# Performance work log

Hardware: AMD Instinct MI355X
Metric: run time of the kernel (lower is better)

Reference implementation:

```python
import jax, jax.numpy as jnp
import numpy as np

N_USERS = 100_000
N_ITEMS = 50_000
N = N_USERS + N_ITEMS
N_LAYERS = 3
ALPHA = 0.8
D = 64
IMG_D = 4096
TXT_D = 384
N_INTER = 2_000_000  # user-item interactions; symmetric nnz = 2*N_INTER


def setup_inputs() -> dict:
    # --- build symmetric-normalized bipartite adjacency (D^-1/2 A D^-1/2) in numpy ---
    rng = np.random.default_rng(0)
    u = rng.integers(0, N_USERS, N_INTER).astype(np.int32)
    i = (rng.integers(0, N_ITEMS, N_INTER) + N_USERS).astype(np.int32)
    rows = np.concatenate([u, i])
    cols = np.concatenate([i, u])
    deg = np.bincount(rows, minlength=N).astype(np.float32)
    d_inv = np.where(deg > 0, deg ** -0.5, 0.0).astype(np.float32)
    vals = d_inv[rows] * d_inv[cols]

    key = jax.random.key(0)
    ks = jax.random.split(key, 8)
    xav_img = float(np.sqrt(6.0 / (IMG_D + D)))
    xav_txt = float(np.sqrt(6.0 / (TXT_D + D)))
    return {
        "image_feats": jax.random.normal(ks[0], (N_ITEMS, IMG_D), jnp.float32),
        "text_feats": jax.random.normal(ks[1], (N_ITEMS, TXT_D), jnp.float32),
        "image_pref": jax.random.normal(ks[2], (N_USERS, D), jnp.float32),
        "text_pref": jax.random.normal(ks[3], (N_USERS, D), jnp.float32),
        "W_img": jax.random.uniform(ks[4], (IMG_D, D), jnp.float32, -xav_img, xav_img),
        "b_img": jnp.zeros((D,), jnp.float32),
        "W_txt": jax.random.uniform(ks[5], (TXT_D, D), jnp.float32, -xav_txt, xav_txt),
        "b_txt": jnp.zeros((D,), jnp.float32),
        "adj_vals": jnp.asarray(vals),
        "adj_rows": jnp.asarray(rows),
        "adj_cols": jnp.asarray(cols),
    }


def _spmm(rows, cols, vals, x):
    # sparse COO @ dense: out[r] += vals[e] * x[cols[e]]
    return jax.ops.segment_sum(vals[:, None] * x[cols], rows, num_segments=N)


def _l2norm(x):
    # F.normalize(x, dim=1): row-wise L2 with eps clamp
    return x / jnp.clip(jnp.linalg.norm(x, axis=1, keepdims=True), 1e-12)


def reference(image_feats, text_feats, image_pref, text_pref,
              W_img, b_img, W_txt, b_txt, adj_vals, adj_rows, adj_cols):
    img = _l2norm(image_feats @ W_img + b_img)   # [n_items, D]
    txt = _l2norm(text_feats @ W_txt + b_txt)    # [n_items, D]
    ego_i = jnp.concatenate([image_pref, img], axis=0)  # [N, D]
    ego_t = jnp.concatenate([text_pref, txt], axis=0)   # [N, D]
    for _ in range(N_LAYERS):
        ego_i = _spmm(adj_rows, adj_cols, adj_vals, ego_i) + ALPHA * ego_i
        ego_t = _spmm(adj_rows, adj_cols, adj_vals, ego_t) + ALPHA * ego_t
    user_preference = jnp.concatenate([ego_i[:N_USERS], ego_t[:N_USERS]], axis=1)  # [n_users, 2D]
    items = jnp.concatenate([ego_i[N_USERS:], ego_t[N_USERS:]], axis=1)            # [n_items, 2D]
    return user_preference, items
```

## Files before the change

### kernel.cpp

```cpp
#include <hip/hip_runtime.h>
#include <hip/hip_bf16.h>

#define N_USERS 100000
#define N_ITEMS 50000
#define N_TOTAL 150000
#define NNZ     4000000
#define ALPHA_F 0.8f
#define ELL_CAP 128

#define G_GEMM 782
#define G_COPY 256
#define G_SCAT 1024
#define NC_IMG 64
#define NC_ALL 70

typedef __attribute__((ext_vector_type(8))) short bf16x8;
typedef __attribute__((ext_vector_type(4))) float f32x4;

static __device__ __forceinline__ short f2bf(float f) {
    unsigned u = __builtin_bit_cast(unsigned, f);
    unsigned r = (u + 0x7fff + ((u >> 16) & 1)) >> 16;
    return (short)r;
}
static __device__ __forceinline__ unsigned pack_bf2(float a, float b) {
    return (unsigned)(unsigned short)f2bf(a) | ((unsigned)(unsigned short)f2bf(b) << 16);
}
static __device__ __forceinline__ float bf_lo(unsigned u) { return __uint_as_float(u << 16); }
static __device__ __forceinline__ float bf_hi(unsigned u) { return __uint_as_float(u & 0xFFFF0000u); }

static __device__ __forceinline__ void gload_lds16(const void* src, void* dst) {
    __builtin_amdgcn_global_load_lds(
        (const __attribute__((address_space(1))) unsigned*)src,
        (__attribute__((address_space(3))) unsigned*)dst, 16, 0, 0);
}


__global__ __launch_bounds__(256) void prep_kernel(const float* __restrict__ Wimg,
                                                   const float* __restrict__ Wtxt,
                                                   int* __restrict__ cnt,
                                                   short* __restrict__ Wti,
                                                   short* __restrict__ Wtt) {
    const int T0 = N_TOTAL;
    const int T1 = T0 + 4096 * 64;
    const int T2 = T1 + 384 * 64;
    int i = blockIdx.x * 256 + threadIdx.x;
    int stride = gridDim.x * 256;
    for (; i < T2; i += stride) {
        if (i < T0) {
            cnt[i] = 0;
        } else if (i < T1) {
            int idx = i - T0; int k = idx >> 6, n = idx & 63;
            Wti[(size_t)n * 4096 + k] = f2bf(Wimg[(size_t)k * 64 + n]);
        } else {
            int idx = i - T1; int k = idx >> 6, n = idx & 63;
            Wtt[(size_t)n * 384 + k] = f2bf(Wtxt[(size_t)k * 64 + n]);
        }
    }
}


static __device__ __forceinline__ void compute_chunk(
        const float* at, const short* bt, int wave, int lane,
        f32x4& c0, f32x4& c1, f32x4& c2, f32x4& c3) {
    const int col = lane & 15, kb = lane >> 4;
    const int arow = 16 * wave + col;
    const char* abase = (const char*)at + arow * 256;
    const int aswz = (arow & 7) << 4;
    const int bswz = (col & 7) << 4;
    const char* bb = (const char*)bt;
    #pragma unroll
    for (int ks = 0; ks < 2; ++ks) {
        int Xa = ks * 128 + kb * 32;
        float4 a0v = *(const float4*)(abase + ((Xa)      ^ aswz));
        float4 a1v = *(const float4*)(abase + ((Xa + 16) ^ aswz));
        bf16x8 af;
        af[0]=f2bf(a0v.x); af[1]=f2bf(a0v.y); af[2]=f2bf(a0v.z); af[3]=f2bf(a0v.w);
        af[4]=f2bf(a1v.x); af[5]=f2bf(a1v.y); af[6]=f2bf(a1v.z); af[7]=f2bf(a1v.w);
        int xb = (ks * 64 + kb * 16) ^ bswz;
        bf16x8 b0 = *(const bf16x8*)(bb + (col +  0) * 128 + xb);
        bf16x8 b1 = *(const bf16x8*)(bb + (col + 16) * 128 + xb);
        bf16x8 b2 = *(const bf16x8*)(bb + (col + 32) * 128 + xb);
        bf16x8 b3 = *(const bf16x8*)(bb + (col + 48) * 128 + xb);
        c0 = __builtin_amdgcn_mfma_f32_16x16x32_bf16(af, b0, c0, 0, 0, 0);
        c1 = __builtin_amdgcn_mfma_f32_16x16x32_bf16(af, b1, c1, 0, 0, 0);
        c2 = __builtin_amdgcn_mfma_f32_16x16x32_bf16(af, b2, c2, 0, 0, 0);
        c3 = __builtin_amdgcn_mfma_f32_16x16x32_bf16(af, b3, c3, 0, 0, 0);
    }
}


__global__ __launch_bounds__(256) void mega_kernel(
        const float* __restrict__ Aimg, const float* __restrict__ Atxt,
        const short* __restrict__ Wti, const short* __restrict__ Wtt,
        const float* __restrict__ bimg, const float* __restrict__ btxt,
        unsigned* __restrict__ egob,
        const int* __restrict__ rows, const int* __restrict__ cols,
        const float* __restrict__ vals, int* __restrict__ cnt, int2* __restrict__ ell,
        const float* __restrict__ img_pref, const float* __restrict__ txt_pref) {
    __shared__ __align__(16) float atile[2][64 * 64];
    __shared__ __align__(16) short btile[2][64 * 64];
    int b = blockIdx.x;
    int t = threadIdx.x;
    int wave = t >> 6, lane = t & 63;
    if (b < G_GEMM) {
        const int row0 = b * 64;
        const int gmax = N_ITEMS - 1;
        const int col = lane & 15, kb = lane >> 4;

        auto stageA = [&](const float* A, int K, int k0, int bi) {
            #pragma unroll
            for (int c = 0; c < 4; ++c) {
                int g = c * 4 + wave;
                int r = g * 4 + (lane >> 4);
                int gr = row0 + r; gr = gr > gmax ? gmax : gr;
                int boff = ((lane & 15) * 16) ^ ((r & 7) << 4);
                const char* src = (const char*)A + ((size_t)gr * K + k0) * 4 + boff;
                char* dst = (char*)&atile[bi][0] + g * 1024 + lane * 16;
                gload_lds16(src, dst);
            }
        };
        auto stageB = [&](const short* W, int K, int k0, int bi) {
            #pragma unroll
            for (int c = 0; c < 2; ++c) {
                int g = c * 4 + wave;
                int bc = g * 8 + (lane >> 3);
                int boff = ((lane & 7) * 16) ^ ((bc & 7) << 4);
                const char* src = (const char*)W + ((size_t)bc * K + k0) * 2 + boff;
                char* dst = (char*)&btile[bi][0] + g * 1024 + lane * 16;
                gload_lds16(src, dst);
            }
        };
        auto stage = [&](int ci, int bi) {
            if (ci < NC_IMG) { stageA(Aimg, 4096, ci * 64, bi); stageB(Wti, 4096, ci * 64, bi); }
            else { stageA(Atxt, 384, (ci - NC_IMG) * 64, bi); stageB(Wtt, 384, (ci - NC_IMG) * 64, bi); }
        };

        f32x4 z = {0.f,0.f,0.f,0.f};
        f32x4 ai0 = z, ai1 = z, ai2 = z, ai3 = z;
        f32x4 at0 = z, at1 = z, at2 = z, at3 = z;

        stage(0, 0);
        for (int ci = 0; ci < NC_ALL; ++ci) {
            int bi = ci & 1;
            if (ci + 1 < NC_ALL) {
                stage(ci + 1, bi ^ 1);
                asm volatile("s_waitcnt vmcnt(6)" ::: "memory");
            } else {
                asm volatile("s_waitcnt vmcnt(0)" ::: "memory");
            }
            __builtin_amdgcn_s_barrier();
            __builtin_amdgcn_sched_barrier(0);
            if (ci < NC_IMG) compute_chunk(&atile[bi][0], &btile[bi][0], wave, lane, ai0, ai1, ai2, ai3);
            else             compute_chunk(&atile[bi][0], &btile[bi][0], wave, lane, at0, at1, at2, at3);
            asm volatile("" ::: "memory");
            __builtin_amdgcn_s_barrier();
            __builtin_amdgcn_sched_barrier(0);
        }

        float bi0 = bimg[ 0 + col], bi1 = bimg[16 + col], bi2 = bimg[32 + col], bi3 = bimg[48 + col];
        float bt0 = btxt[ 0 + col], bt1 = btxt[16 + col], bt2 = btxt[32 + col], bt3 = btxt[48 + col];
        #pragma unroll
        for (int i = 0; i < 4; ++i) {
            ai0[i] += bi0; ai1[i] += bi1; ai2[i] += bi2; ai3[i] += bi3;
            at0[i] += bt0; at1[i] += bt1; at2[i] += bt2; at3[i] += bt3;
        }
        unsigned* egob_items = egob + (size_t)N_USERS * 64;
        #pragma unroll
        for (int i = 0; i < 4; ++i) {
            float ssi = ai0[i]*ai0[i] + ai1[i]*ai1[i] + ai2[i]*ai2[i] + ai3[i]*ai3[i];
            float sst = at0[i]*at0[i] + at1[i]*at1[i] + at2[i]*at2[i] + at3[i]*at3[i];
            #pragma unroll
            for (int off = 1; off < 16; off <<= 1) {
                ssi += __shfl_xor(ssi, off, 64);
                sst += __shfl_xor(sst, off, 64);
            }
            float rni = 1.0f / fmaxf(sqrtf(ssi), 1e-12f);
            float rnt = 1.0f / fmaxf(sqrtf(sst), 1e-12f);
            int r = row0 + 16 * wave + kb * 4 + i;
            if (r < N_ITEMS) {
                unsigned* ob = egob_items + (size_t)r * 64 + col;
                ob[ 0] = pack_bf2(ai0[i]*rni, at0[i]*rnt);
                ob[16] = pack_bf2(ai1[i]*rni, at1[i]*rnt);
                ob[32] = pack_bf2(ai2[i]*rni, at2[i]*rnt);
                ob[48] = pack_bf2(ai3[i]*rni, at3[i]*rnt);
            }
        }
    } else if (b < G_GEMM + G_COPY) {
        int idx = (b - G_GEMM) * 256 + t;
        int stride = G_COPY * 256;
        for (; idx < N_USERS * 16; idx += stride) {
            int row = idx >> 4, w4 = (idx & 15) << 2;
            float4 iv = *reinterpret_cast<const float4*>(&img_pref[(size_t)row * 64 + w4]);
            float4 tv = *reinterpret_cast<const float4*>(&txt_pref[(size_t)row * 64 + w4]);
            uint4 m;
            m.x = pack_bf2(iv.x, tv.x); m.y = pack_bf2(iv.y, tv.y);
            m.z = pack_bf2(iv.z, tv.z); m.w = pack_bf2(iv.w, tv.w);
            *reinterpret_cast<uint4*>(&egob[(size_t)row * 64 + w4]) = m;
        }
    } else {
        int i = (b - G_GEMM - G_COPY) * 256 + t;
        int stride = G_SCAT * 256;
        for (; i < NNZ; i += stride) {
            int r = rows[i];
            int p = atomicAdd(&cnt[r], 1);
            if (p < ELL_CAP)
                ell[(size_t)r * ELL_CAP + p] = make_int2(cols[i], __float_as_int(vals[i]));
        }
    }
}


__global__ __launch_bounds__(256) void spmm_sort_kernel(
        const int* __restrict__ cnt, int2* __restrict__ ell,
        const unsigned* __restrict__ xb, unsigned* __restrict__ outb) {
    __shared__ __align__(16) int2 srt[4][ELL_CAP];
    int wid = threadIdx.x >> 6, lane = threadIdx.x & 63;
    int row = blockIdx.x * 4 + wid;
    bool valid = row < N_TOTAL;
    int deg = 0;
    int2* base = nullptr;
    int2 e0 = make_int2(0x7FFFFFFF, 0), e1 = e0;
    if (valid) {
        deg = min(cnt[row], ELL_CAP);
        base = ell + (size_t)row * ELL_CAP;
        if (lane < deg)      e0 = base[lane];
        if (lane + 64 < deg) e1 = base[lane + 64];
    }
    #pragma unroll
    for (int k = 2; k <= 128; k <<= 1) {
        #pragma unroll
        for (int j = 64; j >= 1; j >>= 1) {
            if (j >= k) continue;
            if (j == 64) {
                if (e0.x > e1.x) { int2 tmp = e0; e0 = e1; e1 = tmp; }
            } else {
                int2 p0, p1;
                p0.x = __shfl_xor(e0.x, j, 64); p0.y = __shfl_xor(e0.y, j, 64);
                p1.x = __shfl_xor(e1.x, j, 64); p1.y = __shfl_xor(e1.y, j, 64);
                bool up0 = ((lane & k) == 0);
                bool up1 = (((lane + 64) & k) == 0);
                bool lo0 = ((lane & j) == 0);
                bool keepmin0 = (up0 == lo0);
                bool keepmin1 = (up1 == lo0);
                if (keepmin0 ? (e0.x > p0.x) : (e0.x < p0.x)) e0 = p0;
                if (keepmin1 ? (e1.x > p1.x) : (e1.x < p1.x)) e1 = p1;
            }
        }
    }
    if (valid) {
        if (lane < deg)      base[lane]      = e0;
        if (lane + 64 < deg) base[lane + 64] = e1;
    }
    srt[wid][lane] = e0;
    srt[wid][lane + 64] = e1;
    __syncthreads();
    if (!valid) return;
    unsigned sw = xb[(size_t)row * 64 + lane];
    float2 acc;
    acc.x = ALPHA_F * bf_lo(sw);
    acc.y = ALPHA_F * bf_hi(sw);
    const int2* s = srt[wid];
    int i = 0;
    for (; i + 8 <= deg; i += 8) {
        int4 p0 = *reinterpret_cast<const int4*>(s + i);
        int4 p1 = *reinterpret_cast<const int4*>(s + i + 2);
        int4 p2 = *reinterpret_cast<const int4*>(s + i + 4);
        int4 p3 = *reinterpret_cast<const int4*>(s + i + 6);
        unsigned g0 = xb[(size_t)p0.x * 64 + lane];
        unsigned g1 = xb[(size_t)p0.z * 64 + lane];
        unsigned g2 = xb[(size_t)p1.x * 64 + lane];
        unsigned g3 = xb[(size_t)p1.z * 64 + lane];
        unsigned g4 = xb[(size_t)p2.x * 64 + lane];
        unsigned g5 = xb[(size_t)p2.z * 64 + lane];
        unsigned g6 = xb[(size_t)p3.x * 64 + lane];
        unsigned g7 = xb[(size_t)p3.z * 64 + lane];
        float v0 = __int_as_float(p0.y), v1 = __int_as_float(p0.w);
        float v2 = __int_as_float(p1.y), v3 = __int_as_float(p1.w);
        float v4 = __int_as_float(p2.y), v5 = __int_as_float(p2.w);
        float v6 = __int_as_float(p3.y), v7 = __int_as_float(p3.w);
        acc.x = fmaf(v0, bf_lo(g0), acc.x); acc.y = fmaf(v0, bf_hi(g0), acc.y);
        acc.x = fmaf(v1, bf_lo(g1), acc.x); acc.y = fmaf(v1, bf_hi(g1), acc.y);
        acc.x = fmaf(v2, bf_lo(g2), acc.x); acc.y = fmaf(v2, bf_hi(g2), acc.y);
        acc.x = fmaf(v3, bf_lo(g3), acc.x); acc.y = fmaf(v3, bf_hi(g3), acc.y);
        acc.x = fmaf(v4, bf_lo(g4), acc.x); acc.y = fmaf(v4, bf_hi(g4), acc.y);
        acc.x = fmaf(v5, bf_lo(g5), acc.x); acc.y = fmaf(v5, bf_hi(g5), acc.y);
        acc.x = fmaf(v6, bf_lo(g6), acc.x); acc.y = fmaf(v6, bf_hi(g6), acc.y);
        acc.x = fmaf(v7, bf_lo(g7), acc.x); acc.y = fmaf(v7, bf_hi(g7), acc.y);
    }
    for (; i < deg; ++i) {
        int2 c = s[i];
        float v = __int_as_float(c.y);
        unsigned g = xb[(size_t)c.x * 64 + lane];
        acc.x = fmaf(v, bf_lo(g), acc.x);
        acc.y = fmaf(v, bf_hi(g), acc.y);
    }
    outb[(size_t)row * 64 + lane] = pack_bf2(acc.x, acc.y);
}


__global__ __launch_bounds__(256) void spmm_kernel(
        const int* __restrict__ cnt, const int2* __restrict__ ell,
        const unsigned* __restrict__ xb,
        float* __restrict__ out32, unsigned* __restrict__ outb) {
    int row = blockIdx.x * 4 + (threadIdx.x >> 6);
    if (row >= N_TOTAL) return;
    int lane = threadIdx.x & 63;
    unsigned sw = xb[(size_t)row * 64 + lane];
    float2 acc;
    acc.x = ALPHA_F * bf_lo(sw);
    acc.y = ALPHA_F * bf_hi(sw);
    int deg = min(cnt[row], ELL_CAP);
    const int2* base = ell + (size_t)row * ELL_CAP;
    int i = 0;
    for (; i + 8 <= deg; i += 8) {
        int4 p0 = *reinterpret_cast<const int4*>(base + i);
        int4 p1 = *reinterpret_cast<const int4*>(base + i + 2);
        int4 p2 = *reinterpret_cast<const int4*>(base + i + 4);
        int4 p3 = *reinterpret_cast<const int4*>(base + i + 6);
        unsigned g0 = xb[(size_t)p0.x * 64 + lane];
        unsigned g1 = xb[(size_t)p0.z * 64 + lane];
        unsigned g2 = xb[(size_t)p1.x * 64 + lane];
        unsigned g3 = xb[(size_t)p1.z * 64 + lane];
        unsigned g4 = xb[(size_t)p2.x * 64 + lane];
        unsigned g5 = xb[(size_t)p2.z * 64 + lane];
        unsigned g6 = xb[(size_t)p3.x * 64 + lane];
        unsigned g7 = xb[(size_t)p3.z * 64 + lane];
        float v0 = __int_as_float(p0.y), v1 = __int_as_float(p0.w);
        float v2 = __int_as_float(p1.y), v3 = __int_as_float(p1.w);
        float v4 = __int_as_float(p2.y), v5 = __int_as_float(p2.w);
        float v6 = __int_as_float(p3.y), v7 = __int_as_float(p3.w);
        acc.x = fmaf(v0, bf_lo(g0), acc.x); acc.y = fmaf(v0, bf_hi(g0), acc.y);
        acc.x = fmaf(v1, bf_lo(g1), acc.x); acc.y = fmaf(v1, bf_hi(g1), acc.y);
        acc.x = fmaf(v2, bf_lo(g2), acc.x); acc.y = fmaf(v2, bf_hi(g2), acc.y);
        acc.x = fmaf(v3, bf_lo(g3), acc.x); acc.y = fmaf(v3, bf_hi(g3), acc.y);
        acc.x = fmaf(v4, bf_lo(g4), acc.x); acc.y = fmaf(v4, bf_hi(g4), acc.y);
        acc.x = fmaf(v5, bf_lo(g5), acc.x); acc.y = fmaf(v5, bf_hi(g5), acc.y);
        acc.x = fmaf(v6, bf_lo(g6), acc.x); acc.y = fmaf(v6, bf_hi(g6), acc.y);
        acc.x = fmaf(v7, bf_lo(g7), acc.x); acc.y = fmaf(v7, bf_hi(g7), acc.y);
    }
    for (; i < deg; ++i) {
        int2 c = base[i];
        float v = __int_as_float(c.y);
        unsigned g = xb[(size_t)c.x * 64 + lane];
        acc.x = fmaf(v, bf_lo(g), acc.x);
        acc.y = fmaf(v, bf_hi(g), acc.y);
    }
    if (out32) {
        out32[(size_t)row * 128 + lane] = acc.x;
        out32[(size_t)row * 128 + 64 + lane] = acc.y;
    }
    if (outb)
        outb[(size_t)row * 64 + lane] = pack_bf2(acc.x, acc.y);
}


extern "C" void kernel_launch(void* const* d_in, const int* in_sizes, int n_in,
                              void* d_out, int out_size, void* d_ws, size_t ws_size,
                              hipStream_t stream) {
    const float* image_feats = (const float*)d_in[0];
    const float* text_feats  = (const float*)d_in[1];
    const float* image_pref  = (const float*)d_in[2];
    const float* text_pref   = (const float*)d_in[3];
    const float* W_img       = (const float*)d_in[4];
    const float* b_img       = (const float*)d_in[5];
    const float* W_txt       = (const float*)d_in[6];
    const float* b_txt       = (const float*)d_in[7];
    const float* adj_vals    = (const float*)d_in[8];
    const int*   adj_rows    = (const int*)d_in[9];
    const int*   adj_cols    = (const int*)d_in[10];

    float* out = (float*)d_out;

    char* ws = (char*)d_ws;
    size_t off = 0;
    auto alloc = [&](size_t bytes) { char* p = ws + off; off += (bytes + 255) & ~size_t(255); return p; };
    int*      cnt    = (int*)     alloc(N_TOTAL * sizeof(int));
    int2*     ell    = (int2*)    alloc((size_t)N_TOTAL * ELL_CAP * sizeof(int2));
    unsigned* m0     = (unsigned*)alloc((size_t)N_TOTAL * 64 * sizeof(unsigned));
    unsigned* m1     = (unsigned*)alloc((size_t)N_TOTAL * 64 * sizeof(unsigned));
    short*    Wt_img = (short*)   alloc((size_t)64 * 4096 * sizeof(short));
    short*    Wt_txt = (short*)   alloc((size_t)64 * 384 * sizeof(short));
    (void)ws_size; (void)out_size; (void)n_in; (void)in_sizes;

    prep_kernel<<<512, 256, 0, stream>>>(W_img, W_txt, cnt, Wt_img, Wt_txt);

    mega_kernel<<<G_GEMM + G_COPY + G_SCAT, 256, 0, stream>>>(
        image_feats, text_feats, Wt_img, Wt_txt, b_img, b_txt, m0,
        adj_rows, adj_cols, adj_vals, cnt, ell, image_pref, text_pref);

    const int ROW_GRID = (N_TOTAL + 3) / 4;
    spmm_sort_kernel<<<ROW_GRID, 256, 0, stream>>>(cnt, ell, m0, m1);
    spmm_kernel<<<ROW_GRID, 256, 0, stream>>>(cnt, ell, m1, nullptr, m0);
    spmm_kernel<<<ROW_GRID, 256, 0, stream>>>(cnt, ell, m0, out, nullptr);
}
```

Baseline: 995.7 us.

## Retile projection GEMM to 16-row blocks with weights read from global

```diff
diff --git a/kernel.cpp b/kernel.cpp
--- a/kernel.cpp
+++ b/kernel.cpp
@@ -8,11 +8,10 @@
 #define ALPHA_F 0.8f
 #define ELL_CAP 128
 
-#define G_GEMM 782
-#define G_COPY 256
-#define G_SCAT 1024
-#define NC_IMG 64
-#define NC_ALL 70
+#define G_SCAT 256
+#define G_COPY 128
+#define G_PRE  (G_SCAT + G_COPY)
+#define G_GEMM 3125
 
 typedef __attribute__((ext_vector_type(8))) short bf16x8;
 typedef __attribute__((ext_vector_type(4))) float f32x4;
@@ -59,37 +58,7 @@
 }
 
 
-static __device__ __forceinline__ void compute_chunk(
-        const float* at, const short* bt, int wave, int lane,
-        f32x4& c0, f32x4& c1, f32x4& c2, f32x4& c3) {
-    const int col = lane & 15, kb = lane >> 4;
-    const int arow = 16 * wave + col;
-    const char* abase = (const char*)at + arow * 256;
-    const int aswz = (arow & 7) << 4;
-    const int bswz = (col & 7) << 4;
-    const char* bb = (const char*)bt;
-    #pragma unroll
-    for (int ks = 0; ks < 2; ++ks) {
-        int Xa = ks * 128 + kb * 32;
-        float4 a0v = *(const float4*)(abase + ((Xa)      ^ aswz));
-        float4 a1v = *(const float4*)(abase + ((Xa + 16) ^ aswz));
-        bf16x8 af;
-        af[0]=f2bf(a0v.x); af[1]=f2bf(a0v.y); af[2]=f2bf(a0v.z); af[3]=f2bf(a0v.w);
-        af[4]=f2bf(a1v.x); af[5]=f2bf(a1v.y); af[6]=f2bf(a1v.z); af[7]=f2bf(a1v.w);
-        int xb = (ks * 64 + kb * 16) ^ bswz;
-        bf16x8 b0 = *(const bf16x8*)(bb + (col +  0) * 128 + xb);
-        bf16x8 b1 = *(const bf16x8*)(bb + (col + 16) * 128 + xb);
-        bf16x8 b2 = *(const bf16x8*)(bb + (col + 32) * 128 + xb);
-        bf16x8 b3 = *(const bf16x8*)(bb + (col + 48) * 128 + xb);
-        c0 = __builtin_amdgcn_mfma_f32_16x16x32_bf16(af, b0, c0, 0, 0, 0);
-        c1 = __builtin_amdgcn_mfma_f32_16x16x32_bf16(af, b1, c1, 0, 0, 0);
-        c2 = __builtin_amdgcn_mfma_f32_16x16x32_bf16(af, b2, c2, 0, 0, 0);
-        c3 = __builtin_amdgcn_mfma_f32_16x16x32_bf16(af, b3, c3, 0, 0, 0);
-    }
-}
-
-
-__global__ __launch_bounds__(256) void mega_kernel(
+__global__ __launch_bounds__(256, 4) void mega_kernel(
         const float* __restrict__ Aimg, const float* __restrict__ Atxt,
         const short* __restrict__ Wti, const short* __restrict__ Wtt,
         const float* __restrict__ bimg, const float* __restrict__ btxt,
@@ -97,96 +66,24 @@
         const int* __restrict__ rows, const int* __restrict__ cols,
         const float* __restrict__ vals, int* __restrict__ cnt, int2* __restrict__ ell,
         const float* __restrict__ img_pref, const float* __restrict__ txt_pref) {
-    __shared__ __align__(16) float atile[2][64 * 64];
-    __shared__ __align__(16) short btile[2][64 * 64];
+    __shared__ __align__(16) char atile[32768];
     int b = blockIdx.x;
     int t = threadIdx.x;
     int wave = t >> 6, lane = t & 63;
-    if (b < G_GEMM) {
-        const int row0 = b * 64;
-        const int gmax = N_ITEMS - 1;
-        const int col = lane & 15, kb = lane >> 4;
-
-        auto stageA = [&](const float* A, int K, int k0, int bi) {
-            #pragma unroll
-            for (int c = 0; c < 4; ++c) {
-                int g = c * 4 + wave;
-                int r = g * 4 + (lane >> 4);
-                int gr = row0 + r; gr = gr > gmax ? gmax : gr;
-                int boff = ((lane & 15) * 16) ^ ((r & 7) << 4);
-                const char* src = (const char*)A + ((size_t)gr * K + k0) * 4 + boff;
-                char* dst = (char*)&atile[bi][0] + g * 1024 + lane * 16;
-                gload_lds16(src, dst);
-            }
-        };
-        auto stageB = [&](const short* W, int K, int k0, int bi) {
-            #pragma unroll
-            for (int c = 0; c < 2; ++c) {
-                int g = c * 4 + wave;
-                int bc = g * 8 + (lane >> 3);
-                int boff = ((lane & 7) * 16) ^ ((bc & 7) << 4);
-                const char* src = (const char*)W + ((size_t)bc * K + k0) * 2 + boff;
-                char* dst = (char*)&btile[bi][0] + g * 1024 + lane * 16;
-                gload_lds16(src, dst);
-            }
-        };
-        auto stage = [&](int ci, int bi) {
-            if (ci < NC_IMG) { stageA(Aimg, 4096, ci * 64, bi); stageB(Wti, 4096, ci * 64, bi); }
-            else { stageA(Atxt, 384, (ci - NC_IMG) * 64, bi); stageB(Wtt, 384, (ci - NC_IMG) * 64, bi); }
-        };
-
-        f32x4 z = {0.f,0.f,0.f,0.f};
-        f32x4 ai0 = z, ai1 = z, ai2 = z, ai3 = z;
-        f32x4 at0 = z, at1 = z, at2 = z, at3 = z;
-
-        stage(0, 0);
-        for (int ci = 0; ci < NC_ALL; ++ci) {
-            int bi = ci & 1;
-            if (ci + 1 < NC_ALL) {
-                stage(ci + 1, bi ^ 1);
-                asm volatile("s_waitcnt vmcnt(6)" ::: "memory");
-            } else {
-                asm volatile("s_waitcnt vmcnt(0)" ::: "memory");
-            }
-            __builtin_amdgcn_s_barrier();
-            __builtin_amdgcn_sched_barrier(0);
-            if (ci < NC_IMG) compute_chunk(&atile[bi][0], &btile[bi][0], wave, lane, ai0, ai1, ai2, ai3);
-            else             compute_chunk(&atile[bi][0], &btile[bi][0], wave, lane, at0, at1, at2, at3);
-            asm volatile("" ::: "memory");
-            __builtin_amdgcn_s_barrier();
-            __builtin_amdgcn_sched_barrier(0);
-        }
-
-        float bi0 = bimg[ 0 + col], bi1 = bimg[16 + col], bi2 = bimg[32 + col], bi3 = bimg[48 + col];
-        float bt0 = btxt[ 0 + col], bt1 = btxt[16 + col], bt2 = btxt[32 + col], bt3 = btxt[48 + col];
-        #pragma unroll
-        for (int i = 0; i < 4; ++i) {
-            ai0[i] += bi0; ai1[i] += bi1; ai2[i] += bi2; ai3[i] += bi3;
-            at0[i] += bt0; at1[i] += bt1; at2[i] += bt2; at3[i] += bt3;
-        }
-        unsigned* egob_items = egob + (size_t)N_USERS * 64;
-        #pragma unroll
-        for (int i = 0; i < 4; ++i) {
-            float ssi = ai0[i]*ai0[i] + ai1[i]*ai1[i] + ai2[i]*ai2[i] + ai3[i]*ai3[i];
-            float sst = at0[i]*at0[i] + at1[i]*at1[i] + at2[i]*at2[i] + at3[i]*at3[i];
-            #pragma unroll
-            for (int off = 1; off < 16; off <<= 1) {
-                ssi += __shfl_xor(ssi, off, 64);
-                sst += __shfl_xor(sst, off, 64);
-            }
-            float rni = 1.0f / fmaxf(sqrtf(ssi), 1e-12f);
-            float rnt = 1.0f / fmaxf(sqrtf(sst), 1e-12f);
-            int r = row0 + 16 * wave + kb * 4 + i;
-            if (r < N_ITEMS) {
-                unsigned* ob = egob_items + (size_t)r * 64 + col;
-                ob[ 0] = pack_bf2(ai0[i]*rni, at0[i]*rnt);
-                ob[16] = pack_bf2(ai1[i]*rni, at1[i]*rnt);
-                ob[32] = pack_bf2(ai2[i]*rni, at2[i]*rnt);
-                ob[48] = pack_bf2(ai3[i]*rni, at3[i]*rnt);
-            }
-        }
-    } else if (b < G_GEMM + G_COPY) {
-        int idx = (b - G_GEMM) * 256 + t;
+
+    if (b < G_SCAT) {
+        int i = b * 256 + t;
+        int stride = G_SCAT * 256;
+        for (; i < NNZ; i += stride) {
+            int r = rows[i];
+            int p = atomicAdd(&cnt[r], 1);
+            if (p < ELL_CAP)
+                ell[(size_t)r * ELL_CAP + p] = make_int2(cols[i], __float_as_int(vals[i]));
+        }
+        return;
+    }
+    if (b < G_PRE) {
+        int idx = (b - G_SCAT) * 256 + t;
         int stride = G_COPY * 256;
         for (; idx < N_USERS * 16; idx += stride) {
             int row = idx >> 4, w4 = (idx & 15) << 2;
@@ -197,15 +94,127 @@
             m.z = pack_bf2(iv.z, tv.z); m.w = pack_bf2(iv.w, tv.w);
             *reinterpret_cast<uint4*>(&egob[(size_t)row * 64 + w4]) = m;
         }
-    } else {
-        int i = (b - G_GEMM - G_COPY) * 256 + t;
-        int stride = G_SCAT * 256;
-        for (; i < NNZ; i += stride) {
-            int r = rows[i];
-            int p = atomicAdd(&cnt[r], 1);
-            if (p < ELL_CAP)
-                ell[(size_t)r * ELL_CAP + p] = make_int2(cols[i], __float_as_int(vals[i]));
-        }
+        return;
+    }
+
+    const int blk = b - G_PRE;
+    const int row0 = blk * 16;
+    const int col = lane & 15, kb = lane >> 4;
+
+    auto stage_img = [&](int ci, int bi) {
+        #pragma unroll
+        for (int j = 0; j < 4; ++j) {
+            int r = wave * 4 + j;
+            int swz = (r & 7) << 4;
+            const char* src = (const char*)Aimg + (size_t)(row0 + r) * 16384
+                              + ci * 1024 + ((lane * 16) ^ swz);
+            char* dst = (char*)atile + bi * 16384 + r * 1024;
+            gload_lds16(src, dst);
+        }
+    };
+    auto stage_txt1 = [&](int bi) {
+        #pragma unroll
+        for (int j = 0; j < 4; ++j) {
+            int r = wave * 4 + j;
+            int swz = (r & 7) << 4;
+            const char* src = (const char*)Atxt + (size_t)(row0 + r) * 1536
+                              + ((lane * 16) ^ swz);
+            char* dst = (char*)atile + bi * 16384 + r * 1024;
+            gload_lds16(src, dst);
+        }
+    };
+    auto stage_txt2 = [&](int bi) {
+        #pragma unroll
+        for (int j = 0; j < 2; ++j) {
+            int p = wave * 2 + j;
+            int r = p * 2 + (lane >> 5);
+            int swz = (r & 7) << 4;
+            const char* src = (const char*)Atxt + (size_t)(row0 + r) * 1536
+                              + 1024 + (((lane & 31) * 16) ^ swz);
+            char* dst = (char*)atile + bi * 16384 + p * 1024;
+            gload_lds16(src, dst);
+        }
+    };
+    auto comp = [&](const char* base, int rstride, const short* Wt, int K, int kabs,
+                    int nks, f32x4& acc) {
+        const int row = col;
+        const int swz = (row & 7) << 4;
+        const char* ab = base + row * rstride;
+        const short* wp = Wt + (size_t)(16 * wave + col) * K + kabs + kb * 8;
+        for (int ks = 0; ks < nks; ++ks) {
+            int lg = kb * 32 + ks * 128;
+            float4 a0 = *(const float4*)(ab + (lg ^ swz));
+            float4 a1 = *(const float4*)(ab + ((lg + 16) ^ swz));
+            bf16x8 af;
+            af[0]=f2bf(a0.x); af[1]=f2bf(a0.y); af[2]=f2bf(a0.z); af[3]=f2bf(a0.w);
+            af[4]=f2bf(a1.x); af[5]=f2bf(a1.y); af[6]=f2bf(a1.z); af[7]=f2bf(a1.w);
+            bf16x8 bf = *(const bf16x8*)(wp + ks * 32);
+            acc = __builtin_amdgcn_mfma_f32_16x16x32_bf16(af, bf, acc, 0, 0, 0);
+        }
+    };
+
+    f32x4 ai = {0.f,0.f,0.f,0.f}, at4 = {0.f,0.f,0.f,0.f};
+
+    stage_img(0, 0);
+    for (int ci = 0; ci < 16; ++ci) {
+        int bi = ci & 1;
+        if (ci < 15) stage_img(ci + 1, bi ^ 1);
+        else         stage_txt1(bi ^ 1);
+        asm volatile("s_waitcnt vmcnt(4)" ::: "memory");
+        __builtin_amdgcn_s_barrier();
+        __builtin_amdgcn_sched_barrier(0);
+        comp((const char*)atile + bi * 16384, 1024, Wti, 4096, ci * 256, 8, ai);
+        asm volatile("" ::: "memory");
+        __builtin_amdgcn_s_barrier();
+        __builtin_amdgcn_sched_barrier(0);
+    }
+    stage_txt2(1);
+    asm volatile("s_waitcnt vmcnt(2)" ::: "memory");
+    __builtin_amdgcn_s_barrier();
+    __builtin_amdgcn_sched_barrier(0);
+    comp((const char*)atile, 1024, Wtt, 384, 0, 8, at4);
+    asm volatile("s_waitcnt vmcnt(0)" ::: "memory");
+    __builtin_amdgcn_s_barrier();
+    __builtin_amdgcn_sched_barrier(0);
+    comp((const char*)atile + 16384, 512, Wtt, 384, 256, 4, at4);
+
+    float bv_i = bimg[16 * wave + col];
+    float bv_t = btxt[16 * wave + col];
+    float ssi[4], sst[4];
+    #pragma unroll
+    for (int i = 0; i < 4; ++i) {
+        ai[i] += bv_i; at4[i] += bv_t;
+        ssi[i] = ai[i] * ai[i];
+        sst[i] = at4[i] * at4[i];
+    }
+    #pragma unroll
+    for (int off = 1; off < 16; off <<= 1) {
+        #pragma unroll
+        for (int i = 0; i < 4; ++i) {
+            ssi[i] += __shfl_xor(ssi[i], off, 64);
+            sst[i] += __shfl_xor(sst[i], off, 64);
+        }
+    }
+    float* S = (float*)atile;
+    __syncthreads();
+    if (col == 0) {
+        #pragma unroll
+        for (int i = 0; i < 4; ++i) {
+            S[wave * 16 + kb * 4 + i]      = ssi[i];
+            S[64 + wave * 16 + kb * 4 + i] = sst[i];
+        }
+    }
+    __syncthreads();
+    unsigned* egob_items = egob + (size_t)N_USERS * 64;
+    #pragma unroll
+    for (int i = 0; i < 4; ++i) {
+        int r = kb * 4 + i;
+        float ti = S[r] + S[16 + r] + S[32 + r] + S[48 + r];
+        float tt = S[64 + r] + S[80 + r] + S[96 + r] + S[112 + r];
+        float rni = 1.0f / fmaxf(sqrtf(ti), 1e-12f);
+        float rnt = 1.0f / fmaxf(sqrtf(tt), 1e-12f);
+        egob_items[(size_t)(row0 + r) * 64 + 16 * wave + col] =
+            pack_bf2(ai[i] * rni, at4[i] * rnt);
     }
 }
 
@@ -384,7 +393,7 @@
 
     prep_kernel<<<512, 256, 0, stream>>>(W_img, W_txt, cnt, Wt_img, Wt_txt);
 
-    mega_kernel<<<G_GEMM + G_COPY + G_SCAT, 256, 0, stream>>>(
+    mega_kernel<<<G_PRE + G_GEMM, 256, 0, stream>>>(
         image_feats, text_feats, Wt_img, Wt_txt, b_img, b_txt, m0,
         adj_rows, adj_cols, adj_vals, cnt, ell, image_pref, text_pref);
 
```

Measured after the change: 976.3 us. No clear change (-1.9%).

## Reorder mega kernel blocks, pre-tile swizzled weights, add occupancy hint

Applied to the files above, without the earlier changes.

```diff
diff --git a/kernel.cpp b/kernel.cpp
--- a/kernel.cpp
+++ b/kernel.cpp
@@ -8,9 +8,10 @@
 #define ALPHA_F 0.8f
 #define ELL_CAP 128
 
+#define G_SCAT 1024
+#define G_COPY 128
+#define G_PRE  (G_SCAT + G_COPY)
 #define G_GEMM 782
-#define G_COPY 256
-#define G_SCAT 1024
 #define NC_IMG 64
 #define NC_ALL 70
 
@@ -38,8 +39,8 @@
 __global__ __launch_bounds__(256) void prep_kernel(const float* __restrict__ Wimg,
                                                    const float* __restrict__ Wtxt,
                                                    int* __restrict__ cnt,
-                                                   short* __restrict__ Wti,
-                                                   short* __restrict__ Wtt) {
+                                                   char* __restrict__ WtiT,
+                                                   char* __restrict__ WttT) {
     const int T0 = N_TOTAL;
     const int T1 = T0 + 4096 * 64;
     const int T2 = T1 + 384 * 64;
@@ -50,143 +51,46 @@
             cnt[i] = 0;
         } else if (i < T1) {
             int idx = i - T0; int k = idx >> 6, n = idx & 63;
-            Wti[(size_t)n * 4096 + k] = f2bf(Wimg[(size_t)k * 64 + n]);
+            int c = k >> 6, kk = k & 63;
+            *(short*)(WtiT + c * 8192 + n * 128 + ((kk * 2) ^ ((n & 7) << 4)))
+                = f2bf(Wimg[(size_t)k * 64 + n]);
         } else {
             int idx = i - T1; int k = idx >> 6, n = idx & 63;
-            Wtt[(size_t)n * 384 + k] = f2bf(Wtxt[(size_t)k * 64 + n]);
-        }
-    }
-}
-
-
-static __device__ __forceinline__ void compute_chunk(
-        const float* at, const short* bt, int wave, int lane,
-        f32x4& c0, f32x4& c1, f32x4& c2, f32x4& c3) {
-    const int col = lane & 15, kb = lane >> 4;
-    const int arow = 16 * wave + col;
-    const char* abase = (const char*)at + arow * 256;
-    const int aswz = (arow & 7) << 4;
-    const int bswz = (col & 7) << 4;
-    const char* bb = (const char*)bt;
-    #pragma unroll
-    for (int ks = 0; ks < 2; ++ks) {
-        int Xa = ks * 128 + kb * 32;
-        float4 a0v = *(const float4*)(abase + ((Xa)      ^ aswz));
-        float4 a1v = *(const float4*)(abase + ((Xa + 16) ^ aswz));
-        bf16x8 af;
-        af[0]=f2bf(a0v.x); af[1]=f2bf(a0v.y); af[2]=f2bf(a0v.z); af[3]=f2bf(a0v.w);
-        af[4]=f2bf(a1v.x); af[5]=f2bf(a1v.y); af[6]=f2bf(a1v.z); af[7]=f2bf(a1v.w);
-        int xb = (ks * 64 + kb * 16) ^ bswz;
-        bf16x8 b0 = *(const bf16x8*)(bb + (col +  0) * 128 + xb);
-        bf16x8 b1 = *(const bf16x8*)(bb + (col + 16) * 128 + xb);
-        bf16x8 b2 = *(const bf16x8*)(bb + (col + 32) * 128 + xb);
-        bf16x8 b3 = *(const bf16x8*)(bb + (col + 48) * 128 + xb);
-        c0 = __builtin_amdgcn_mfma_f32_16x16x32_bf16(af, b0, c0, 0, 0, 0);
-        c1 = __builtin_amdgcn_mfma_f32_16x16x32_bf16(af, b1, c1, 0, 0, 0);
-        c2 = __builtin_amdgcn_mfma_f32_16x16x32_bf16(af, b2, c2, 0, 0, 0);
-        c3 = __builtin_amdgcn_mfma_f32_16x16x32_bf16(af, b3, c3, 0, 0, 0);
-    }
-}
-
-
-__global__ __launch_bounds__(256) void mega_kernel(
+            int c = k >> 6, kk = k & 63;
+            *(short*)(WttT + c * 8192 + n * 128 + ((kk * 2) ^ ((n & 7) << 4)))
+                = f2bf(Wtxt[(size_t)k * 64 + n]);
+        }
+    }
+}
+
+
+__global__ __launch_bounds__(256, 3) void mega_kernel(
         const float* __restrict__ Aimg, const float* __restrict__ Atxt,
-        const short* __restrict__ Wti, const short* __restrict__ Wtt,
+        const char* __restrict__ WtiT, const char* __restrict__ WttT,
         const float* __restrict__ bimg, const float* __restrict__ btxt,
         unsigned* __restrict__ egob,
         const int* __restrict__ rows, const int* __restrict__ cols,
         const float* __restrict__ vals, int* __restrict__ cnt, int2* __restrict__ ell,
         const float* __restrict__ img_pref, const float* __restrict__ txt_pref) {
-    __shared__ __align__(16) float atile[2][64 * 64];
-    __shared__ __align__(16) short btile[2][64 * 64];
+    __shared__ __align__(16) char abuf[2][16384];
+    __shared__ __align__(16) char bbuf[2][8192];
     int b = blockIdx.x;
     int t = threadIdx.x;
     int wave = t >> 6, lane = t & 63;
-    if (b < G_GEMM) {
-        const int row0 = b * 64;
-        const int gmax = N_ITEMS - 1;
-        const int col = lane & 15, kb = lane >> 4;
-
-        auto stageA = [&](const float* A, int K, int k0, int bi) {
-            #pragma unroll
-            for (int c = 0; c < 4; ++c) {
-                int g = c * 4 + wave;
-                int r = g * 4 + (lane >> 4);
-                int gr = row0 + r; gr = gr > gmax ? gmax : gr;
-                int boff = ((lane & 15) * 16) ^ ((r & 7) << 4);
-                const char* src = (const char*)A + ((size_t)gr * K + k0) * 4 + boff;
-                char* dst = (char*)&atile[bi][0] + g * 1024 + lane * 16;
-                gload_lds16(src, dst);
-            }
-        };
-        auto stageB = [&](const short* W, int K, int k0, int bi) {
-            #pragma unroll
-            for (int c = 0; c < 2; ++c) {
-                int g = c * 4 + wave;
-                int bc = g * 8 + (lane >> 3);
-                int boff = ((lane & 7) * 16) ^ ((bc & 7) << 4);
-                const char* src = (const char*)W + ((size_t)bc * K + k0) * 2 + boff;
-                char* dst = (char*)&btile[bi][0] + g * 1024 + lane * 16;
-                gload_lds16(src, dst);
-            }
-        };
-        auto stage = [&](int ci, int bi) {
-            if (ci < NC_IMG) { stageA(Aimg, 4096, ci * 64, bi); stageB(Wti, 4096, ci * 64, bi); }
-            else { stageA(Atxt, 384, (ci - NC_IMG) * 64, bi); stageB(Wtt, 384, (ci - NC_IMG) * 64, bi); }
-        };
-
-        f32x4 z = {0.f,0.f,0.f,0.f};
-        f32x4 ai0 = z, ai1 = z, ai2 = z, ai3 = z;
-        f32x4 at0 = z, at1 = z, at2 = z, at3 = z;
-
-        stage(0, 0);
-        for (int ci = 0; ci < NC_ALL; ++ci) {
-            int bi = ci & 1;
-            if (ci + 1 < NC_ALL) {
-                stage(ci + 1, bi ^ 1);
-                asm volatile("s_waitcnt vmcnt(6)" ::: "memory");
-            } else {
-                asm volatile("s_waitcnt vmcnt(0)" ::: "memory");
-            }
-            __builtin_amdgcn_s_barrier();
-            __builtin_amdgcn_sched_barrier(0);
-            if (ci < NC_IMG) compute_chunk(&atile[bi][0], &btile[bi][0], wave, lane, ai0, ai1, ai2, ai3);
-            else             compute_chunk(&atile[bi][0], &btile[bi][0], wave, lane, at0, at1, at2, at3);
-            asm volatile("" ::: "memory");
-            __builtin_amdgcn_s_barrier();
-            __builtin_amdgcn_sched_barrier(0);
-        }
-
-        float bi0 = bimg[ 0 + col], bi1 = bimg[16 + col], bi2 = bimg[32 + col], bi3 = bimg[48 + col];
-        float bt0 = btxt[ 0 + col], bt1 = btxt[16 + col], bt2 = btxt[32 + col], bt3 = btxt[48 + col];
-        #pragma unroll
-        for (int i = 0; i < 4; ++i) {
-            ai0[i] += bi0; ai1[i] += bi1; ai2[i] += bi2; ai3[i] += bi3;
-            at0[i] += bt0; at1[i] += bt1; at2[i] += bt2; at3[i] += bt3;
-        }
-        unsigned* egob_items = egob + (size_t)N_USERS * 64;
-        #pragma unroll
-        for (int i = 0; i < 4; ++i) {
-            float ssi = ai0[i]*ai0[i] + ai1[i]*ai1[i] + ai2[i]*ai2[i] + ai3[i]*ai3[i];
-            float sst = at0[i]*at0[i] + at1[i]*at1[i] + at2[i]*at2[i] + at3[i]*at3[i];
-            #pragma unroll
-            for (int off = 1; off < 16; off <<= 1) {
-                ssi += __shfl_xor(ssi, off, 64);
-                sst += __shfl_xor(sst, off, 64);
-            }
-            float rni = 1.0f / fmaxf(sqrtf(ssi), 1e-12f);
-            float rnt = 1.0f / fmaxf(sqrtf(sst), 1e-12f);
-            int r = row0 + 16 * wave + kb * 4 + i;
-            if (r < N_ITEMS) {
-                unsigned* ob = egob_items + (size_t)r * 64 + col;
-                ob[ 0] = pack_bf2(ai0[i]*rni, at0[i]*rnt);
-                ob[16] = pack_bf2(ai1[i]*rni, at1[i]*rnt);
-                ob[32] = pack_bf2(ai2[i]*rni, at2[i]*rnt);
-                ob[48] = pack_bf2(ai3[i]*rni, at3[i]*rnt);
-            }
-        }
-    } else if (b < G_GEMM + G_COPY) {
-        int idx = (b - G_GEMM) * 256 + t;
+
+    if (b < G_SCAT) {
+        int i = b * 256 + t;
+        int stride = G_SCAT * 256;
+        for (; i < NNZ; i += stride) {
+            int r = rows[i];
+            int p = atomicAdd(&cnt[r], 1);
+            if (p < ELL_CAP)
+                ell[(size_t)r * ELL_CAP + p] = make_int2(cols[i], __float_as_int(vals[i]));
+        }
+        return;
+    }
+    if (b < G_PRE) {
+        int idx = (b - G_SCAT) * 256 + t;
         int stride = G_COPY * 256;
         for (; idx < N_USERS * 16; idx += stride) {
             int row = idx >> 4, w4 = (idx & 15) << 2;
@@ -197,14 +101,108 @@
             m.z = pack_bf2(iv.z, tv.z); m.w = pack_bf2(iv.w, tv.w);
             *reinterpret_cast<uint4*>(&egob[(size_t)row * 64 + w4]) = m;
         }
-    } else {
-        int i = (b - G_GEMM - G_COPY) * 256 + t;
-        int stride = G_SCAT * 256;
-        for (; i < NNZ; i += stride) {
-            int r = rows[i];
-            int p = atomicAdd(&cnt[r], 1);
-            if (p < ELL_CAP)
-                ell[(size_t)r * ELL_CAP + p] = make_int2(cols[i], __float_as_int(vals[i]));
+        return;
+    }
+
+    const int blk = b - G_PRE;
+    const int row0 = blk * 64;
+    const int col = lane & 15, kb = lane >> 4;
+    const int gmax = N_ITEMS - 1;
+
+    auto stage = [&](int ci, int bi) {
+        const float* A; size_t rowbytes; const char* BT; int cc;
+        if (ci < NC_IMG) { A = Aimg; rowbytes = 16384; BT = WtiT; cc = ci; }
+        else             { A = Atxt; rowbytes = 1536;  BT = WttT; cc = ci - NC_IMG; }
+        #pragma unroll
+        for (int q = 0; q < 4; ++q) {
+            int g = q * 4 + wave;
+            int r = g * 4 + (lane >> 4);
+            int gr = row0 + r; gr = gr > gmax ? gmax : gr;
+            int so = ((lane & 15) * 16) ^ ((r & 7) << 4);
+            const char* src = (const char*)A + (size_t)gr * rowbytes + cc * 256 + so;
+            char* dst = abuf[bi] + g * 1024 + lane * 16;
+            gload_lds16(src, dst);
+        }
+        #pragma unroll
+        for (int q = 0; q < 2; ++q) {
+            int off = (q * 4 + wave) * 1024 + lane * 16;
+            gload_lds16(BT + (size_t)cc * 8192 + off, bbuf[bi] + off);
+        }
+    };
+
+    auto comp = [&](int bi, f32x4& c0, f32x4& c1, f32x4& c2, f32x4& c3) {
+        const int arow = 16 * wave + col;
+        const int aswz = (arow & 7) << 4;
+        const char* ab = abuf[bi] + arow * 256;
+        const char* bb = bbuf[bi];
+        const int bswz = (col & 7) << 4;
+        #pragma unroll
+        for (int ks = 0; ks < 2; ++ks) {
+            int la = ks * 128 + kb * 32;
+            float4 a0 = *(const float4*)(ab + (la ^ aswz));
+            float4 a1 = *(const float4*)(ab + ((la + 16) ^ aswz));
+            bf16x8 af;
+            af[0]=f2bf(a0.x); af[1]=f2bf(a0.y); af[2]=f2bf(a0.z); af[3]=f2bf(a0.w);
+            af[4]=f2bf(a1.x); af[5]=f2bf(a1.y); af[6]=f2bf(a1.z); af[7]=f2bf(a1.w);
+            int kByte = (ks * 64 + kb * 16) ^ bswz;
+            bf16x8 b0 = *(const bf16x8*)(bb + (col +  0) * 128 + kByte);
+            bf16x8 b1 = *(const bf16x8*)(bb + (col + 16) * 128 + kByte);
+            bf16x8 b2 = *(const bf16x8*)(bb + (col + 32) * 128 + kByte);
+            bf16x8 b3 = *(const bf16x8*)(bb + (col + 48) * 128 + kByte);
+            c0 = __builtin_amdgcn_mfma_f32_16x16x32_bf16(af, b0, c0, 0, 0, 0);
+            c1 = __builtin_amdgcn_mfma_f32_16x16x32_bf16(af, b1, c1, 0, 0, 0);
+            c2 = __builtin_amdgcn_mfma_f32_16x16x32_bf16(af, b2, c2, 0, 0, 0);
+            c3 = __builtin_amdgcn_mfma_f32_16x16x32_bf16(af, b3, c3, 0, 0, 0);
+        }
+    };
+
+    f32x4 z = {0.f,0.f,0.f,0.f};
+    f32x4 ai0 = z, ai1 = z, ai2 = z, ai3 = z;
+    f32x4 at0 = z, at1 = z, at2 = z, at3 = z;
+
+    stage(0, 0);
+    for (int ci = 0; ci < NC_ALL; ++ci) {
+        int bi = ci & 1;
+        if (ci + 1 < NC_ALL) {
+            stage(ci + 1, bi ^ 1);
+            asm volatile("s_waitcnt vmcnt(6)" ::: "memory");
+        } else {
+            asm volatile("s_waitcnt vmcnt(0)" ::: "memory");
+        }
+        __builtin_amdgcn_s_barrier();
+        __builtin_amdgcn_sched_barrier(0);
+        if (ci < NC_IMG) comp(bi, ai0, ai1, ai2, ai3);
+        else             comp(bi, at0, at1, at2, at3);
+        __builtin_amdgcn_sched_barrier(0);
+        __builtin_amdgcn_s_barrier();
+    }
+
+    float bi0 = bimg[ 0 + col], bi1 = bimg[16 + col], bi2 = bimg[32 + col], bi3 = bimg[48 + col];
+    float bt0 = btxt[ 0 + col], bt1 = btxt[16 + col], bt2 = btxt[32 + col], bt3 = btxt[48 + col];
+    #pragma unroll
+    for (int i = 0; i < 4; ++i) {
+        ai0[i] += bi0; ai1[i] += bi1; ai2[i] += bi2; ai3[i] += bi3;
+        at0[i] += bt0; at1[i] += bt1; at2[i] += bt2; at3[i] += bt3;
+    }
+    unsigned* egob_items = egob + (size_t)N_USERS * 64;
+    #pragma unroll
+    for (int i = 0; i < 4; ++i) {
+        float ssi = ai0[i]*ai0[i] + ai1[i]*ai1[i] + ai2[i]*ai2[i] + ai3[i]*ai3[i];
+        float sst = at0[i]*at0[i] + at1[i]*at1[i] + at2[i]*at2[i] + at3[i]*at3[i];
+        #pragma unroll
+        for (int off = 1; off < 16; off <<= 1) {
+            ssi += __shfl_xor(ssi, off, 64);
+            sst += __shfl_xor(sst, off, 64);
+        }
+        float rni = 1.0f / fmaxf(sqrtf(ssi), 1e-12f);
+        float rnt = 1.0f / fmaxf(sqrtf(sst), 1e-12f);
+        int r = row0 + 16 * wave + kb * 4 + i;
+        if (r < N_ITEMS) {
+            unsigned* ob = egob_items + (size_t)r * 64 + col;
+            ob[ 0] = pack_bf2(ai0[i]*rni, at0[i]*rnt);
+            ob[16] = pack_bf2(ai1[i]*rni, at1[i]*rnt);
+            ob[32] = pack_bf2(ai2[i]*rni, at2[i]*rnt);
+            ob[48] = pack_bf2(ai3[i]*rni, at3[i]*rnt);
         }
     }
 }
@@ -374,18 +372,18 @@
     char* ws = (char*)d_ws;
     size_t off = 0;
     auto alloc = [&](size_t bytes) { char* p = ws + off; off += (bytes + 255) & ~size_t(255); return p; };
-    int*      cnt    = (int*)     alloc(N_TOTAL * sizeof(int));
-    int2*     ell    = (int2*)    alloc((size_t)N_TOTAL * ELL_CAP * sizeof(int2));
-    unsigned* m0     = (unsigned*)alloc((size_t)N_TOTAL * 64 * sizeof(unsigned));
-    unsigned* m1     = (unsigned*)alloc((size_t)N_TOTAL * 64 * sizeof(unsigned));
-    short*    Wt_img = (short*)   alloc((size_t)64 * 4096 * sizeof(short));
-    short*    Wt_txt = (short*)   alloc((size_t)64 * 384 * sizeof(short));
+    int*      cnt   = (int*)     alloc(N_TOTAL * sizeof(int));
+    int2*     ell   = (int2*)    alloc((size_t)N_TOTAL * ELL_CAP * sizeof(int2));
+    unsigned* m0    = (unsigned*)alloc((size_t)N_TOTAL * 64 * sizeof(unsigned));
+    unsigned* m1    = (unsigned*)alloc((size_t)N_TOTAL * 64 * sizeof(unsigned));
+    char*     WtiT  = (char*)    alloc((size_t)NC_IMG * 8192);
+    char*     WttT  = (char*)    alloc((size_t)6 * 8192);
     (void)ws_size; (void)out_size; (void)n_in; (void)in_sizes;
 
-    prep_kernel<<<512, 256, 0, stream>>>(W_img, W_txt, cnt, Wt_img, Wt_txt);
-
-    mega_kernel<<<G_GEMM + G_COPY + G_SCAT, 256, 0, stream>>>(
-        image_feats, text_feats, Wt_img, Wt_txt, b_img, b_txt, m0,
+    prep_kernel<<<512, 256, 0, stream>>>(W_img, W_txt, cnt, WtiT, WttT);
+
+    mega_kernel<<<G_PRE + G_GEMM, 256, 0, stream>>>(
+        image_feats, text_feats, WtiT, WttT, b_img, b_txt, m0,
         adj_rows, adj_cols, adj_vals, cnt, ell, image_pref, text_pref);
 
     const int ROW_GRID = (N_TOTAL + 3) / 4;
```

Result: no change. 1.015 ms (+1.9%).
